# Optimization experiments

Hardware: AMD Instinct MI355X
Metric: run time of the kernel (lower is better)

The kernel has to match this reference:

```python
import jax, jax.numpy as jnp
import numpy as np

EPS = 1e-8
NU_MOLECULAR = 1.5e-05
# loss weights (module defaults)
DATA_W, BC_W, TURB_W, RANS_W, SMOOTH_W, WALL_W = 1.0, 0.05, 0.05, 0.05, 0.01, 0.02
CONT_INIT = CONT_TGT = 0.1
MOM_INIT = MOM_TGT = 0.1
RAMP_STEPS, RAMP_START = 1000, 0

N_NODES, N_EDGES = 100000, 6400000


def _curriculum_weights(step):
    if step < RAMP_START:
        return CONT_INIT, MOM_INIT
    if step >= RAMP_START + RAMP_STEPS:
        return CONT_TGT, MOM_TGT
    alpha = (step - RAMP_START) / RAMP_STEPS  # linear ramp
    return ((1 - alpha) * CONT_INIT + alpha * CONT_TGT,
            (1 - alpha) * MOM_INIT + alpha * MOM_TGT)


def setup_inputs() -> dict:
    key = jax.random.key(0)
    k1, k2, k3, k4, k5 = jax.random.split(key, 5)
    predictions = jax.random.normal(k1, (N_NODES, 4), dtype=jnp.float32)
    targets = jax.random.normal(k2, (N_NODES, 4), dtype=jnp.float32)
    # dx, dy strictly positive edge offsets
    edge_attr_dxdy = jax.random.uniform(k3, (N_EDGES, 2), dtype=jnp.float32, minval=1e-3, maxval=0.05)
    edge_index = jax.random.randint(k4, (2, N_EDGES), 0, N_NODES, dtype=jnp.int64)
    wall_mask = jax.random.bernoulli(k5, 0.05, (N_NODES,))
    return {"predictions": predictions, "targets": targets,
            "edge_attr_dxdy": edge_attr_dxdy, "edge_index": edge_index,
            "wall_mask": wall_mask, "step": 500}


def reference(predictions, targets, edge_attr_dxdy, edge_index, wall_mask, step):
    cont_w, mom_w = _curriculum_weights(int(step))
    N = predictions.shape[0]
    row, col = edge_index[0], edge_index[1]
    u, v, p, nu_t = (predictions[:, i] for i in range(4))
    dx, dy = edge_attr_dxdy[:, 0], edge_attr_dxdy[:, 1]

    # per-edge finite differences (single gather of node fields)
    du = u[col] - u[row]
    dv = v[col] - v[row]
    dp = p[col] - p[row]

    seg = lambda e: jax.ops.segment_sum(e, row, num_segments=N)
    edge_count = jnp.maximum(seg(jnp.ones_like(du)), 1.0)

    # --- data loss ---
    mse_loss = jnp.mean((predictions - targets) ** 2)

    # --- continuity (divergence) loss ---
    divergence = (seg(du / (dx + EPS)) + seg(dv / (dy + EPS))) / edge_count
    div_loss = jnp.mean(divergence ** 2)

    # --- momentum loss ---
    p_grad_x = seg(dp / (dx + EPS)) / edge_count
    p_grad_y = seg(dp / (dy + EPS)) / edge_count
    lap_u = seg(du / (dx ** 2 + EPS)) / edge_count
    lap_v = seg(dv / (dy ** 2 + EPS)) / edge_count
    nu_eff = NU_MOLECULAR + nu_t
    momentum_loss = jnp.mean((p_grad_x + nu_eff * lap_u) ** 2 +
                             (p_grad_y + nu_eff * lap_v) ** 2)

    # --- turbulence losses ---
    positivity_loss = jnp.mean(jax.nn.relu(-nu_t) ** 2)
    du_dx = du / (dx + EPS)
    du_dy = du / (dy + EPS)
    dv_dx = dv / (dx + EPS)
    dv_dy = dv / (dy + EPS)
    strain_sq_edge = 2.0 * (du_dx ** 2 + dv_dy ** 2) + (du_dy + dv_dx) ** 2
    strain_node = seg(strain_sq_edge) / edge_count
    production = nu_t * strain_node
    turb_production_loss = jnp.mean(production ** 2)
    turb_dissipation_loss = jnp.mean(nu_t ** 2)

    # --- boundary-condition & wall-function losses (wall mask) ---
    m = wall_mask.astype(u.dtype)
    n_wall = jnp.maximum(jnp.sum(m), 1.0)
    bc_loss = jnp.sum(m * (u ** 2 + v ** 2)) / n_wall
    wall_loss = jnp.sum(m * (u ** 2 + v ** 2 + nu_t ** 2)) / n_wall

    # --- smoothness loss over edges ---
    smooth_loss = jnp.mean((predictions[col] - predictions[row]) ** 2)

    total = (DATA_W * mse_loss + cont_w * div_loss + mom_w * momentum_loss +
             TURB_W * turb_production_loss + RANS_W * turb_dissipation_loss +
             BC_W * bc_loss + SMOOTH_W * smooth_loss + WALL_W * wall_loss)
    # positivity_loss is tracked but not weighted into total (per visible code paths)
    return total
```

## Files before the change

kernel.cpp:

```cpp
#include <hip/hip_runtime.h>
#include <hip/hip_fp16.h>

#define EPS 1e-8f
#define NU_MOL 1.5e-5f
#define NPB 512
#define MAXNB 256
#define NBP 256
#define NBLK 4096
#define CMAX 1664
#define KMAX 7
#define CH 1536
#define KACC 3
#define SPLIT 6
#define NGRP 64
#define GRP 64


union U32H2 { unsigned u; __half2 h; };

__device__ inline unsigned packh2(float a, float b) {
    U32H2 x; x.h = __halves2half2(__float2half_rn(a), __float2half_rn(b));
    return x.u;
}
__device__ inline float2 unpackh2(unsigned u) {
    U32H2 x; x.u = u;
    return make_float2(__low2float(x.h), __high2float(x.h));
}

__device__ inline int detect64(const void* eidx, int N) {
    const long long* ll = (const long long*)eidx;
    int is64 = 1;
    #pragma unroll
    for (int i = 0; i < 16; ++i) {
        long long v = ll[i];
        if (v < 0 || v >= (long long)N) is64 = 0;
    }
    return is64;
}


__global__ void detect_idx_dtype(const void* eidx, int N, int* flag) {
    const long long* ll = (const long long*)eidx;
    int is64 = 1;
    for (int i = 0; i < 16; ++i) {
        long long v = ll[i];
        if (v < 0 || v >= (long long)N) { is64 = 0; break; }
    }
    *flag = is64;
}

__global__ void finalize_kernel(const double* __restrict__ d,
                                const double* __restrict__ smooth_slots,
                                int N, int E, float* __restrict__ out)
{
    double smooth = 0.0;
    for (int i = 0; i < 64; ++i) smooth += smooth_slots[i];
    double dN = (double)N;
    double n_wall = d[5] > 1.0 ? d[5] : 1.0;
    double total = 1.0  * d[0] / (4.0 * dN)
                 + 0.1  * d[1] / dN
                 + 0.1  * d[2] / dN
                 + 0.05 * d[3] / dN
                 + 0.05 * d[4] / dN
                 + 0.05 * d[6] / n_wall
                 + 0.01 * smooth / (4.0 * (double)E)
                 + 0.02 * d[7] / n_wall;
    out[0] = (float)total;
}


__global__ __launch_bounds__(256) void count_kernel(
    const void* __restrict__ eidx, int E, int N, int NB,
    unsigned* __restrict__ counts, unsigned* __restrict__ gsum)
{
    __shared__ unsigned hist[4][MAXNB];
    hist[0][threadIdx.x] = 0u;
    hist[1][threadIdx.x] = 0u;
    hist[2][threadIdx.x] = 0u;
    hist[3][threadIdx.x] = 0u;
    __syncthreads();
    const int w = (threadIdx.x >> 6) & 3;
    const int is64 = detect64(eidx, N);
    const long long* ll = (const long long*)eidx;
    const int* ii = (const int*)eidx;
    int chunk = (E + NBLK - 1) / NBLK;
    int s = blockIdx.x * chunk;
    int Cb = min(chunk, E - s);

    unsigned rr[KMAX];
    #pragma unroll
    for (int k = 0; k < KMAX; ++k) {
        int i = k * 256 + threadIdx.x;
        if (i < Cb) {
            int r = is64 ? (int)ll[s + i] : ii[s + i];
            rr[k] = (unsigned)min(max(r, 0), N - 1);
        } else rr[k] = 0xFFFFFFFFu;
    }
    #pragma unroll
    for (int k = 0; k < KMAX; ++k)
        if (rr[k] != 0xFFFFFFFFu)
            atomicAdd(&hist[w][rr[k] >> 9], 1u);
    __syncthreads();
    if (threadIdx.x < NB) {
        unsigned h = hist[0][threadIdx.x] + hist[1][threadIdx.x]
                   + hist[2][threadIdx.x] + hist[3][threadIdx.x];
        counts[(size_t)blockIdx.x * NBP + threadIdx.x] = h;
        if (h) atomicAdd(&gsum[(size_t)(blockIdx.x >> 6) * NBP + threadIdx.x], h);
    }
}

__global__ __launch_bounds__(512) void scan_base_kernel(
    unsigned* __restrict__ gsum, unsigned* __restrict__ base, int NB)
{
    __shared__ unsigned sc[512];
    int t = threadIdx.x;
    unsigned vg[NGRP];
    unsigned total = 0;
    if (t < NB) {
        #pragma unroll
        for (int g = 0; g < NGRP; ++g) {
            vg[g] = gsum[(size_t)g * NBP + t];
            total += vg[g];
        }
    }
    sc[t] = total; __syncthreads();
    for (int off = 1; off < 512; off <<= 1) {
        unsigned x = (t >= off) ? sc[t - off] : 0u;
        __syncthreads();
        sc[t] += x;
        __syncthreads();
    }
    unsigned ex = sc[t] - total;
    if (t < NB) {
        base[t] = ex;
        unsigned run = ex;
        #pragma unroll
        for (int g = 0; g < NGRP; ++g) {
            unsigned x = vg[g];
            gsum[(size_t)g * NBP + t] = run;
            run += x;
        }
    }
    if (t == 511) base[NB] = sc[511];
}

__global__ __launch_bounds__(256) void local_scan_kernel(
    unsigned* __restrict__ counts, const unsigned* __restrict__ gsum, int NB)
{
    __shared__ unsigned segs[4][64];
    int g = blockIdx.x;
    int b0 = blockIdx.y * 64;
    int j = threadIdx.x & 63, seg = threadIdx.x >> 6;
    int b = b0 + j;
    unsigned v[16];
    unsigned ssum = 0;
    if (b < NB) {
        #pragma unroll
        for (int k = 0; k < 16; ++k) {
            int row = g * GRP + seg * 16 + k;
            v[k] = counts[(size_t)row * NBP + b];
            ssum += v[k];
        }
    }
    segs[seg][j] = ssum;
    __syncthreads();
    if (b < NB) {
        unsigned carry = gsum[(size_t)g * NBP + b];
        for (int s_ = 0; s_ < seg; ++s_) carry += segs[s_][j];
        #pragma unroll
        for (int k = 0; k < 16; ++k) {
            int row = g * GRP + seg * 16 + k;
            counts[(size_t)row * NBP + b] = carry;
            carry += v[k];
        }
    }
}

__global__ __launch_bounds__(256) void scatter_kernel(
    const void* __restrict__ eidx, const float2* __restrict__ eattr,
    int E, int N, int NB,
    const unsigned* __restrict__ localoff ,
    uint2* __restrict__ vals)
{
    __shared__ unsigned hist[2][MAXNB];
    __shared__ unsigned cur[MAXNB];
    __shared__ unsigned gb2[MAXNB];
    __shared__ uint2 pl[CMAX];
    __shared__ unsigned char bb[CMAX];
    __shared__ unsigned wt[4];

    const int t = threadIdx.x;
    const int blk = blockIdx.x;
    const int lane = t & 63, wv = t >> 6;
    const int w = wv & 1;
    const int is64 = detect64(eidx, N);
    const long long* ll = (const long long*)eidx;
    const int* ii = (const int*)eidx;
    const int chunk = (E + NBLK - 1) / NBLK;
    const int s = blk * chunk;
    const int Cb = min(chunk, E - s);

    hist[0][t] = 0u;
    hist[1][t] = 0u;
    __syncthreads();

    unsigned rr[KMAX], rk[KMAX];
    #pragma unroll
    for (int k = 0; k < KMAX; ++k) {
        int i = k * 256 + t;
        if (i < Cb) {
            int r = is64 ? (int)ll[s + i] : ii[s + i];
            rr[k] = (unsigned)min(max(r, 0), N - 1);
        } else rr[k] = 0xFFFFFFFFu;
    }
    #pragma unroll
    for (int k = 0; k < KMAX; ++k)
        if (rr[k] != 0xFFFFFFFFu)
            rk[k] = atomicAdd(&hist[w][rr[k] >> 9], 1u);
    if (t < NB) gb2[t] = localoff[(size_t)blk * NBP + t];
    __syncthreads();

    unsigned h = hist[0][t] + hist[1][t];
    unsigned x = h;
    #pragma unroll
    for (int off = 1; off < 64; off <<= 1) {
        unsigned y = (unsigned)__shfl_up((int)x, off, 64);
        if (lane >= off) x += y;
    }
    if (lane == 63) wt[wv] = x;
    __syncthreads();
    unsigned wadd = 0;
    for (int w2 = 0; w2 < wv; ++w2) wadd += wt[w2];
    unsigned ex = x + wadd - h;
    cur[t] = ex;
    __syncthreads();
    if (t < NB) gb2[t] -= cur[t];

    int cc[KMAX]; float2 dd[KMAX];
    #pragma unroll
    for (int k = 0; k < KMAX; ++k) {
        int i = k * 256 + t;
        if (i < Cb) {
            int e = s + i;
            cc[k] = is64 ? (int)ll[(long long)E + e] : ii[E + e];
            dd[k] = eattr[e];
        }
    }
    #pragma unroll
    for (int k = 0; k < KMAX; ++k) {
        int i = k * 256 + t;
        if (i < Cb) {
            unsigned r = rr[k];
            unsigned b = r >> 9;
            unsigned rl = r & (NPB - 1);
            int c = min(max(cc[k], 0), N - 1);
            unsigned slot = cur[b] + (w ? hist[0][b] : 0u) + rk[k];
            pl[slot] = make_uint2((unsigned)c | (rl << 17),
                                  packh2(dd[k].x, dd[k].y));
            bb[slot] = (unsigned char)b;
        }
    }
    __syncthreads();

    uint2 op[KMAX]; unsigned ob[KMAX];
    #pragma unroll
    for (int k = 0; k < KMAX; ++k) {
        int p = k * 256 + t;
        if (p < Cb) { op[k] = pl[p]; ob[k] = (unsigned)bb[p]; }
    }
    #pragma unroll
    for (int k = 0; k < KMAX; ++k) {
        int p = k * 256 + t;
        if (p < Cb) vals[gb2[ob[k]] + (unsigned)p] = op[k];
    }
}

__global__ __launch_bounds__(512) void accum_kernel(
    const uint2* __restrict__ vals, const unsigned* __restrict__ base,
    const float4* __restrict__ pred, int N,
    float* __restrict__ g , double* __restrict__ smooth_slots)
{
    __shared__ float4 pl[CH];
    __shared__ uint2 ph[NPB];
    __shared__ unsigned hist[NPB];
    __shared__ unsigned cur[NPB];
    __shared__ unsigned wt[8];
    __shared__ double sm[8];

    const int b = blockIdx.x;
    const int t = threadIdx.x;
    const int wv = t >> 6, lane = t & 63;
    const int n0 = b * NPB;

    {
        int n = n0 + t;
        float4 p = (n < N) ? pred[n] : make_float4(0.f, 0.f, 0.f, 0.f);
        ph[t] = make_uint2(packh2(p.x, p.y), packh2(p.z, p.w));
    }

    unsigned s0 = base[b], e0 = base[b + 1];
    unsigned len = e0 - s0;
    unsigned s = s0 + (unsigned)(((unsigned long long)len * blockIdx.y) / SPLIT);
    unsigned e = s0 + (unsigned)(((unsigned long long)len * (blockIdx.y + 1)) / SPLIT);

    float cnt = 0, sdiv = 0, smx = 0, smy = 0, sstr = 0;
    double smooth = 0.0;

    for (unsigned cs = s; cs < e; cs += CH) {
        const int n = (int)min((unsigned)CH, e - cs);
        hist[t] = 0u;
        __syncthreads();

        uint2 vv[KACC]; unsigned rk2[KACC]; float4 pcc[KACC];
        #pragma unroll
        for (int k = 0; k < KACC; ++k) {
            int i = k * 512 + t;
            if (i < n) vv[k] = vals[cs + i];
            else vv[k].x = 0xFFFFFFFFu;
        }
        #pragma unroll
        for (int k = 0; k < KACC; ++k) {
            int i = k * 512 + t;
            if (i < n) {
                rk2[k] = atomicAdd(&hist[(vv[k].x >> 17) & (NPB - 1)], 1u);
                pcc[k] = pred[vv[k].x & 0x1FFFFu];
            }
        }
        __syncthreads();

        unsigned v = hist[t];
        unsigned x = v;
        #pragma unroll
        for (int off = 1; off < 64; off <<= 1) {
            unsigned y = (unsigned)__shfl_up((int)x, off, 64);
            if (lane >= off) x += y;
        }
        if (lane == 63) wt[wv] = x;
        __syncthreads();
        unsigned wadd = 0;
        for (int w = 0; w < wv; ++w) wadd += wt[w];
        unsigned incl = x + wadd;
        unsigned ex0 = incl - v;
        cur[t] = ex0;
        cnt += (float)v;
        __syncthreads();

        #pragma unroll
        for (int k = 0; k < KACC; ++k) {
            int i = k * 512 + t;
            if (i >= n) continue;
            unsigned pk = vv[k].x;
            unsigned rl = (pk >> 17) & (NPB - 1);
            float2 dxy = unpackh2(vv[k].y);
            float4 pc = pcc[k];
            uint2 pru = ph[rl];
            float2 pxy = unpackh2(pru.x);
            float2 pzw = unpackh2(pru.y);
            float du = pc.x - pxy.x, dv = pc.y - pxy.y;
            float dp = pc.z - pzw.x, dn = pc.w - pzw.y;
            float rx  = __builtin_amdgcn_rcpf(dxy.x + EPS);
            float ry  = __builtin_amdgcn_rcpf(dxy.y + EPS);
            float rx2 = __builtin_amdgcn_rcpf(dxy.x * dxy.x + EPS);
            float ry2 = __builtin_amdgcn_rcpf(dxy.y * dxy.y + EPS);
            float du_dx = du * rx, du_dy = du * ry;
            float dv_dx = dv * rx, dv_dy = dv * ry;
            float nu_eff = NU_MOL + pzw.y;
            float sh = du_dy + dv_dx;
            float div_e = du_dx + dv_dy;
            float mx_e  = dp * rx + nu_eff * du * rx2;
            float my_e  = dp * ry + nu_eff * dv * ry2;
            float str_e = 2.0f * (du_dx * du_dx + dv_dy * dv_dy) + sh * sh;
            pl[cur[rl] + rk2[k]] = make_float4(div_e, mx_e, my_e, str_e);
            smooth += (double)(du * du + dv * dv + dp * dp + dn * dn);
        }
        __syncthreads();

        for (unsigned i = ex0; i < incl; ++i) {
            float4 pv = pl[i];
            sdiv += pv.x;
            smx  += pv.y;
            smy  += pv.z;
            sstr += pv.w;
        }
        __syncthreads();
    }

    {
        int n = n0 + t;
        if (n < N) {
            atomicAdd(&g[0 * (size_t)N + n], cnt);
            atomicAdd(&g[1 * (size_t)N + n], sdiv);
            atomicAdd(&g[2 * (size_t)N + n], smx);
            atomicAdd(&g[3 * (size_t)N + n], smy);
            atomicAdd(&g[4 * (size_t)N + n], sstr);
        }
    }

    for (int off = 32; off > 0; off >>= 1)
        smooth += __shfl_down(smooth, off);
    if (lane == 0) sm[wv] = smooth;
    __syncthreads();
    if (t == 0) {
        double tot = 0;
        #pragma unroll
        for (int w = 0; w < 8; ++w) tot += sm[w];
        atomicAdd(&smooth_slots[(b * SPLIT + blockIdx.y) & 63], tot);
    }
}

__global__ __launch_bounds__(256) void node_final_kernel(
    const float* __restrict__ g, const float4* __restrict__ pred,
    const float4* __restrict__ tgt, const unsigned char* __restrict__ wall,
    int N, double* __restrict__ d)
{
    int i = blockIdx.x * 256 + threadIdx.x;
    double v0 = 0, v1 = 0, v2 = 0, v3 = 0, v4 = 0, v5 = 0, v6 = 0, v7 = 0;
    if (i < N) {
        float cnt = g[0 * (size_t)N + i];
        float inv = 1.0f / fmaxf(cnt, 1.0f);
        float div = g[1 * (size_t)N + i] * inv;
        float mx  = g[2 * (size_t)N + i] * inv;
        float my  = g[3 * (size_t)N + i] * inv;
        float sn  = g[4 * (size_t)N + i] * inv;
        float4 p = pred[i];
        float4 tg = tgt[i];
        float prod = p.w * sn;
        float m = wall[i] ? 1.0f : 0.0f;
        float e0 = p.x - tg.x, e1 = p.y - tg.y, e2 = p.z - tg.z, e3 = p.w - tg.w;
        float uv = p.x * p.x + p.y * p.y;
        v0 = (double)(e0 * e0 + e1 * e1 + e2 * e2 + e3 * e3);
        v1 = (double)div * (double)div;
        v2 = (double)mx * (double)mx + (double)my * (double)my;
        v3 = (double)prod * (double)prod;
        v4 = (double)p.w * (double)p.w;
        v5 = (double)m;
        v6 = (double)(m * uv);
        v7 = (double)(m * (uv + p.w * p.w));
    }
    for (int off = 32; off > 0; off >>= 1) {
        v0 += __shfl_down(v0, off); v1 += __shfl_down(v1, off);
        v2 += __shfl_down(v2, off); v3 += __shfl_down(v3, off);
        v4 += __shfl_down(v4, off); v5 += __shfl_down(v5, off);
        v6 += __shfl_down(v6, off); v7 += __shfl_down(v7, off);
    }
    __shared__ double sm[4][8];
    int lane = threadIdx.x & 63, wv = threadIdx.x >> 6;
    if (lane == 0) {
        sm[wv][0] = v0; sm[wv][1] = v1; sm[wv][2] = v2; sm[wv][3] = v3;
        sm[wv][4] = v4; sm[wv][5] = v5; sm[wv][6] = v6; sm[wv][7] = v7;
    }
    __syncthreads();
    if (threadIdx.x < 8) {
        int q = threadIdx.x;
        atomicAdd(&d[q], sm[0][q] + sm[1][q] + sm[2][q] + sm[3][q]);
    }
}


__global__ __launch_bounds__(256) void edge_kernel(
    const void* __restrict__ eidx, const float2* __restrict__ eattr,
    const float4* __restrict__ pred, int E, int N, const int* __restrict__ flag,
    float* __restrict__ a_cnt, float* __restrict__ a_div,
    float* __restrict__ a_mx, float* __restrict__ a_my,
    float* __restrict__ a_str, double* __restrict__ smooth_slots)
{
    const int is64 = *flag;
    const long long* ll = (const long long*)eidx;
    const int* ii = (const int*)eidx;
    double smooth = 0.0;
    const int stride = gridDim.x * blockDim.x;
    for (int e = blockIdx.x * blockDim.x + threadIdx.x; e < E; e += stride) {
        int row, col;
        if (is64) { row = (int)ll[e]; col = (int)ll[(long long)E + e]; }
        else      { row = ii[e];      col = ii[E + e]; }
        row = min(max(row, 0), N - 1);
        col = min(max(col, 0), N - 1);
        float2 dxy = eattr[e];
        float4 pr = pred[row];
        float4 pc = pred[col];
        float du = pc.x - pr.x, dv = pc.y - pr.y;
        float dp = pc.z - pr.z, dn = pc.w - pr.w;
        float rx  = 1.0f / (dxy.x + EPS);
        float ry  = 1.0f / (dxy.y + EPS);
        float rx2 = 1.0f / (dxy.x * dxy.x + EPS);
        float ry2 = 1.0f / (dxy.y * dxy.y + EPS);
        float du_dx = du * rx, du_dy = du * ry;
        float dv_dx = dv * rx, dv_dy = dv * ry;
        float nu_eff = NU_MOL + pr.w;
        atomicAdd(&a_cnt[row], 1.0f);
        atomicAdd(&a_div[row], du_dx + dv_dy);
        atomicAdd(&a_mx[row], dp * rx + nu_eff * du * rx2);
        atomicAdd(&a_my[row], dp * ry + nu_eff * dv * ry2);
        float sh = du_dy + dv_dx;
        atomicAdd(&a_str[row], 2.0f * (du_dx * du_dx + dv_dy * dv_dy) + sh * sh);
        smooth += (double)(du * du + dv * dv + dp * dp + dn * dn);
    }
    for (int off = 32; off > 0; off >>= 1)
        smooth += __shfl_down(smooth, off);
    __shared__ double sm[4];
    int lane = threadIdx.x & 63, wv = threadIdx.x >> 6;
    if (lane == 0) sm[wv] = smooth;
    __syncthreads();
    if (threadIdx.x == 0)
        atomicAdd(&smooth_slots[blockIdx.x & 63], sm[0] + sm[1] + sm[2] + sm[3]);
}

__global__ __launch_bounds__(256) void node_kernel(
    const float4* __restrict__ pred, const float4* __restrict__ tgt,
    const unsigned char* __restrict__ wall, int N,
    const float* __restrict__ a_cnt, const float* __restrict__ a_div,
    const float* __restrict__ a_mx, const float* __restrict__ a_my,
    const float* __restrict__ a_str, double* __restrict__ d)
{
    int i = blockIdx.x * blockDim.x + threadIdx.x;
    double v0 = 0, v1 = 0, v2 = 0, v3 = 0, v4 = 0, v5 = 0, v6 = 0, v7 = 0;
    if (i < N) {
        float4 p = pred[i];
        float4 t = tgt[i];
        float inv = 1.0f / fmaxf(a_cnt[i], 1.0f);
        float div = a_div[i] * inv;
        float mx = a_mx[i] * inv, my = a_my[i] * inv;
        float sn = a_str[i] * inv;
        float prod = p.w * sn;
        float m = wall[i] ? 1.0f : 0.0f;
        float e0 = p.x - t.x, e1 = p.y - t.y, e2 = p.z - t.z, e3 = p.w - t.w;
        float uv = p.x * p.x + p.y * p.y;
        v0 = (double)(e0 * e0 + e1 * e1 + e2 * e2 + e3 * e3);
        v1 = (double)div * (double)div;
        v2 = (double)mx * (double)mx + (double)my * (double)my;
        v3 = (double)prod * (double)prod;
        v4 = (double)p.w * (double)p.w;
        v5 = (double)m;
        v6 = (double)(m * uv);
        v7 = (double)(m * (uv + p.w * p.w));
    }
    for (int off = 32; off > 0; off >>= 1) {
        v0 += __shfl_down(v0, off); v1 += __shfl_down(v1, off);
        v2 += __shfl_down(v2, off); v3 += __shfl_down(v3, off);
        v4 += __shfl_down(v4, off); v5 += __shfl_down(v5, off);
        v6 += __shfl_down(v6, off); v7 += __shfl_down(v7, off);
    }
    __shared__ double sm[4][8];
    int lane = threadIdx.x & 63, wv = threadIdx.x >> 6;
    if (lane == 0) {
        sm[wv][0] = v0; sm[wv][1] = v1; sm[wv][2] = v2; sm[wv][3] = v3;
        sm[wv][4] = v4; sm[wv][5] = v5; sm[wv][6] = v6; sm[wv][7] = v7;
    }
    __syncthreads();
    if (threadIdx.x < 8) {
        int q = threadIdx.x;
        atomicAdd(&d[q], sm[0][q] + sm[1][q] + sm[2][q] + sm[3][q]);
    }
}


extern "C" void kernel_launch(void* const* d_in, const int* in_sizes, int n_in,
                              void* d_out, int out_size, void* d_ws, size_t ws_size,
                              hipStream_t stream) {
    const float4* pred = (const float4*)d_in[0];
    const float4* tgt  = (const float4*)d_in[1];
    const float2* eattr = (const float2*)d_in[2];
    const void* eidx = d_in[3];
    const unsigned char* wall = (const unsigned char*)d_in[4];
    int N = in_sizes[0] / 4;
    int E = in_sizes[2] / 2;
    int NB = (N + NPB - 1) / NPB;
    int chunk = (E + NBLK - 1) / NBLK;
    int ntiles = (NB + 63) / 64;

    char* ws = (char*)d_ws;
    double* d = (double*)ws;
    double* smooth_slots = d + 8;
    int* flag = (int*)(ws + 576);

    size_t off = 1024;
    float* g        = (float*)(ws + off);     off += (size_t)5 * N * 4;
    unsigned* gsum   = (unsigned*)(ws + off); off += (size_t)NGRP * NBP * 4;
    size_t zbytes = off;
    unsigned* counts = (unsigned*)(ws + off); off += (size_t)NBLK * NBP * 4;
    unsigned* base   = (unsigned*)(ws + off); off += (size_t)(NB + 1) * 4;
    off = (off + 15) & ~(size_t)15;
    uint2* vals      = (uint2*)(ws + off);    off += (size_t)E * 8;
    size_t need_fast = off;

    bool fast = (NB <= MAXNB) && (N <= 131072) && (chunk <= CMAX) &&
                (ws_size >= need_fast);

    if (fast) {
        hipMemsetAsync(d_ws, 0, zbytes, stream);
        count_kernel<<<NBLK, 256, 0, stream>>>(eidx, E, N, NB, counts, gsum);
        scan_base_kernel<<<1, 512, 0, stream>>>(gsum, base, NB);
        local_scan_kernel<<<dim3(NGRP, ntiles), 256, 0, stream>>>(counts, gsum, NB);
        scatter_kernel<<<NBLK, 256, 0, stream>>>(eidx, eattr, E, N, NB,
                                                 counts, vals);
        accum_kernel<<<dim3(NB, SPLIT), 512, 0, stream>>>(vals, base, pred, N,
                                                          g, smooth_slots);
        node_final_kernel<<<(N + 255) / 256, 256, 0, stream>>>(g, pred, tgt, wall,
                                                               N, d);
        finalize_kernel<<<1, 1, 0, stream>>>(d, smooth_slots, N, E, (float*)d_out);
    } else {
        float* arrays = (float*)(ws + 1024);
        float* a_cnt = arrays + (size_t)0 * N;
        float* a_div = arrays + (size_t)1 * N;
        float* a_mx  = arrays + (size_t)2 * N;
        float* a_my  = arrays + (size_t)3 * N;
        float* a_str = arrays + (size_t)4 * N;
        size_t zb = 1024 + (size_t)5 * N * sizeof(float);
        hipMemsetAsync(d_ws, 0, zb, stream);
        detect_idx_dtype<<<1, 1, 0, stream>>>(eidx, N, flag);
        edge_kernel<<<4096, 256, 0, stream>>>(eidx, eattr, pred, E, N, flag,
                                              a_cnt, a_div, a_mx, a_my, a_str,
                                              smooth_slots);
        node_kernel<<<(N + 255) / 256, 256, 0, stream>>>(pred, tgt, wall, N,
                                                         a_cnt, a_div, a_mx, a_my,
                                                         a_str, d);
        finalize_kernel<<<1, 1, 0, stream>>>(d, smooth_slots, N, E, (float*)d_out);
    }
}
```

Baseline: 236.5 us.

## Cache row keys and per-wave ranks from count pass to skip re-histogramming in scatter

The count kernel now records each edge's clamped row, wave id and atomic rank into a packed 32-bit array, plus the per-wave bucket histograms as 16-bit values. A new scatter kernel reads these back instead of reloading 64-bit row indices and redoing the shared-memory atomic histogram, so slot positions come straight from the saved ranks. This trades a second pass of index reads and shared atomics for an extra E*4-byte write and read plus the histogram traffic, and it needs more workspace. The old path stays as a fallback when the workspace is too small.

```diff
diff --git a/kernel.cpp b/kernel.cpp
--- a/kernel.cpp
+++ b/kernel.cpp
@@ -71,7 +71,8 @@
 
 __global__ __launch_bounds__(256) void count_kernel(
     const void* __restrict__ eidx, int E, int N, int NB,
-    unsigned* __restrict__ counts, unsigned* __restrict__ gsum)
+    unsigned* __restrict__ counts, unsigned* __restrict__ gsum,
+    int pk_en, unsigned* __restrict__ pack, unsigned short* __restrict__ phist)
 {
     __shared__ unsigned hist[4][MAXNB];
     hist[0][threadIdx.x] = 0u;
@@ -87,7 +88,7 @@
     int s = blockIdx.x * chunk;
     int Cb = min(chunk, E - s);
 
-    unsigned rr[KMAX];
+    unsigned rr[KMAX], rk[KMAX];
     #pragma unroll
     for (int k = 0; k < KMAX; ++k) {
         int i = k * 256 + threadIdx.x;
@@ -99,13 +100,29 @@
     #pragma unroll
     for (int k = 0; k < KMAX; ++k)
         if (rr[k] != 0xFFFFFFFFu)
-            atomicAdd(&hist[w][rr[k] >> 9], 1u);
+            rk[k] = atomicAdd(&hist[w][rr[k] >> 9], 1u);
+    if (pk_en) {
+        #pragma unroll
+        for (int k = 0; k < KMAX; ++k) {
+            int i = k * 256 + threadIdx.x;
+            if (i < Cb)
+                pack[s + i] = rr[k] | ((unsigned)w << 17) | (rk[k] << 19);
+        }
+    }
     __syncthreads();
     if (threadIdx.x < NB) {
-        unsigned h = hist[0][threadIdx.x] + hist[1][threadIdx.x]
-                   + hist[2][threadIdx.x] + hist[3][threadIdx.x];
+        unsigned h0 = hist[0][threadIdx.x], h1 = hist[1][threadIdx.x];
+        unsigned h2 = hist[2][threadIdx.x], h3 = hist[3][threadIdx.x];
+        unsigned h = h0 + h1 + h2 + h3;
         counts[(size_t)blockIdx.x * NBP + threadIdx.x] = h;
         if (h) atomicAdd(&gsum[(size_t)(blockIdx.x >> 6) * NBP + threadIdx.x], h);
+        if (pk_en) {
+            unsigned short* pb = phist + (size_t)blockIdx.x * 4 * NBP + threadIdx.x;
+            pb[0 * NBP] = (unsigned short)h0;
+            pb[1 * NBP] = (unsigned short)h1;
+            pb[2 * NBP] = (unsigned short)h2;
+            pb[3 * NBP] = (unsigned short)h3;
+        }
     }
 }
 
@@ -176,10 +193,111 @@
     }
 }
 
+__global__ __launch_bounds__(256) void scatter_pk_kernel(
+    const void* __restrict__ eidx, const float2* __restrict__ eattr,
+    int E, int N, int NB,
+    const unsigned* __restrict__ localoff,
+    const unsigned* __restrict__ pack,
+    const unsigned short* __restrict__ phist,
+    uint2* __restrict__ vals)
+{
+    __shared__ unsigned cur[MAXNB];
+    __shared__ unsigned cp[4][MAXNB];
+    __shared__ unsigned gb2[MAXNB];
+    __shared__ uint2 pl[CMAX];
+    __shared__ unsigned char bb[CMAX];
+    __shared__ unsigned wt[4];
+
+    const int t = threadIdx.x;
+    const int blk = blockIdx.x;
+    const int lane = t & 63, wv = t >> 6;
+    const int is64 = detect64(eidx, N);
+    const long long* ll = (const long long*)eidx;
+    const int* ii = (const int*)eidx;
+    const int chunk = (E + NBLK - 1) / NBLK;
+    const int s = blk * chunk;
+    const int Cb = min(chunk, E - s);
+
+    unsigned pk7[KMAX];
+    #pragma unroll
+    for (int k = 0; k < KMAX; ++k) {
+        int i = k * 256 + t;
+        pk7[k] = (i < Cb) ? pack[s + i] : 0u;
+    }
+    unsigned h = 0;
+    if (t < NB) {
+        const unsigned short* pb = phist + (size_t)blk * 4 * NBP + t;
+        unsigned h0 = pb[0 * NBP], h1 = pb[1 * NBP];
+        unsigned h2 = pb[2 * NBP], h3 = pb[3 * NBP];
+        h = h0 + h1 + h2 + h3;
+        cp[0][t] = 0u;
+        cp[1][t] = h0;
+        cp[2][t] = h0 + h1;
+        cp[3][t] = h0 + h1 + h2;
+        gb2[t] = localoff[(size_t)blk * NBP + t];
+    }
+
+    unsigned x = h;
+    #pragma unroll
+    for (int off = 1; off < 64; off <<= 1) {
+        unsigned y = (unsigned)__shfl_up((int)x, off, 64);
+        if (lane >= off) x += y;
+    }
+    if (lane == 63) wt[wv] = x;
+    __syncthreads();
+    unsigned wadd = 0;
+    for (int w2 = 0; w2 < wv; ++w2) wadd += wt[w2];
+    unsigned ex = x + wadd - h;
+    cur[t] = ex;
+    __syncthreads();
+    if (t < NB) gb2[t] -= cur[t];
+
+    int cc[KMAX]; float2 dd[KMAX];
+    #pragma unroll
+    for (int k = 0; k < KMAX; ++k) {
+        int i = k * 256 + t;
+        if (i < Cb) {
+            int e = s + i;
+            cc[k] = is64 ? (int)ll[(long long)E + e] : ii[E + e];
+            dd[k] = eattr[e];
+        }
+    }
+    #pragma unroll
+    for (int k = 0; k < KMAX; ++k) {
+        int i = k * 256 + t;
+        if (i < Cb) {
+            unsigned pk = pk7[k];
+            unsigned r = pk & 0x1FFFFu;
+            unsigned p = (pk >> 17) & 3u;
+            unsigned rank = pk >> 19;
+            unsigned b = r >> 9;
+            unsigned rl = r & (NPB - 1);
+            int c = min(max(cc[k], 0), N - 1);
+            unsigned slot = cur[b] + cp[p][b] + rank;
+            pl[slot] = make_uint2((unsigned)c | (rl << 17),
+                                  packh2(dd[k].x, dd[k].y));
+            bb[slot] = (unsigned char)b;
+        }
+    }
+    __syncthreads();
+
+    uint2 op[KMAX]; unsigned ob[KMAX];
+    #pragma unroll
+    for (int k = 0; k < KMAX; ++k) {
+        int p = k * 256 + t;
+        if (p < Cb) { op[k] = pl[p]; ob[k] = (unsigned)bb[p]; }
+    }
+    #pragma unroll
+    for (int k = 0; k < KMAX; ++k) {
+        int p = k * 256 + t;
+        if (p < Cb) vals[gb2[ob[k]] + (unsigned)p] = op[k];
+    }
+}
+
 __global__ __launch_bounds__(256) void scatter_kernel(
     const void* __restrict__ eidx, const float2* __restrict__ eattr,
     int E, int N, int NB,
-    const unsigned* __restrict__ localoff ,
+    const unsigned* __restrict__ localoff,
     uint2* __restrict__ vals)
 {
     __shared__ unsigned hist[2][MAXNB];
@@ -582,17 +700,27 @@
     off = (off + 15) & ~(size_t)15;
     uint2* vals      = (uint2*)(ws + off);    off += (size_t)E * 8;
     size_t need_fast = off;
-
-    bool fast = (NB <= MAXNB) && (N <= 131072) && (chunk <= CMAX) &&
-                (ws_size >= need_fast);
-
-    if (fast) {
+    unsigned* pack   = (unsigned*)(ws + off); off += (size_t)E * 4;
+    unsigned short* phist = (unsigned short*)(ws + off);
+    off += (size_t)NBLK * 4 * NBP * 2;
+    size_t need_pk = off;
+
+    bool shape_ok = (NB <= MAXNB) && (N <= 131072) && (chunk <= CMAX);
+    bool fast_pk = shape_ok && (ws_size >= need_pk);
+    bool fast    = shape_ok && (ws_size >= need_fast);
+
+    if (fast_pk || fast) {
         hipMemsetAsync(d_ws, 0, zbytes, stream);
-        count_kernel<<<NBLK, 256, 0, stream>>>(eidx, E, N, NB, counts, gsum);
+        count_kernel<<<NBLK, 256, 0, stream>>>(eidx, E, N, NB, counts, gsum,
+                                               fast_pk ? 1 : 0, pack, phist);
         scan_base_kernel<<<1, 512, 0, stream>>>(gsum, base, NB);
         local_scan_kernel<<<dim3(NGRP, ntiles), 256, 0, stream>>>(counts, gsum, NB);
-        scatter_kernel<<<NBLK, 256, 0, stream>>>(eidx, eattr, E, N, NB,
-                                                 counts, vals);
+        if (fast_pk)
+            scatter_pk_kernel<<<NBLK, 256, 0, stream>>>(eidx, eattr, E, N, NB,
+                                                        counts, pack, phist, vals);
+        else
+            scatter_kernel<<<NBLK, 256, 0, stream>>>(eidx, eattr, E, N, NB,
+                                                     counts, vals);
         accum_kernel<<<dim3(NB, SPLIT), 512, 0, stream>>>(vals, base, pred, N,
                                                           g, smooth_slots);
         node_final_kernel<<<(N + 255) / 256, 256, 0, stream>>>(g, pred, tgt, wall,
```

New measurement: 242.6 us. 1.03x slower.
